# Kernel tuning notes

Measured on AMD Instinct MI355X. Metric: run time of the kernel, lower is better.

Reference implementation:

```python
import jax, jax.numpy as jnp
import numpy as np

B, T, F, U = 256, 1024, 64, 128  # batch, history_size, model_input_num, GRU units


def gru(x_seq, W, Uk, b, return_sequences):
    """Keras GRU (reset_after=True, recurrent_activation=sigmoid, activation=relu).
    x_seq: [B,T,F_in]; W: [F_in,3U]; Uk: [U,3U]; b: [2,3U] (input bias, recurrent bias).
    """
    b_i, b_r = b[0], b[1]
    xw = jnp.einsum('bti,iu->btu', x_seq, W) + b_i  # precompute input projection [B,T,3U]

    def step(h, xw_t):
        rec = h @ Uk + b_r                          # [B,3U]
        xz, xr, xh = jnp.split(xw_t, 3, axis=-1)
        rz, rr, rh = jnp.split(rec, 3, axis=-1)
        z = jax.nn.sigmoid(xz + rz)
        r = jax.nn.sigmoid(xr + rr)
        hh = jax.nn.relu(xh + r * rh)
        h_new = z * h + (1.0 - z) * hh
        return h_new, h_new

    h0 = jnp.zeros((x_seq.shape[0], Uk.shape[0]), dtype=x_seq.dtype)
    hT, hs = jax.lax.scan(step, h0, jnp.swapaxes(xw, 0, 1))  # scan over time
    if return_sequences:
        return jnp.swapaxes(hs, 0, 1), hT  # [B,T,U], [B,U]
    return hT, hT


def setup_inputs() -> dict:
    key = jax.random.key(0)
    ks = jax.random.split(key, 7)
    s_in1 = 1.0 / np.sqrt(F)
    s_rec = 1.0 / np.sqrt(U)
    return {
        'input_data': jax.random.normal(ks[0], (B, T, F), dtype=jnp.float32),
        'W1': jax.random.normal(ks[1], (F, 3 * U), dtype=jnp.float32) * s_in1,
        'U1': jax.random.normal(ks[2], (U, 3 * U), dtype=jnp.float32) * s_rec,
        'b1': jnp.zeros((2, 3 * U), dtype=jnp.float32),
        'W2': jax.random.normal(ks[3], (U, 3 * U), dtype=jnp.float32) * s_rec,
        'U2': jax.random.normal(ks[4], (U, 3 * U), dtype=jnp.float32) * s_rec,
        'b2': jnp.zeros((2, 3 * U), dtype=jnp.float32),
    }


def reference(input_data, W1, U1, b1, W2, U2, b2):
    seq1, state1 = gru(input_data, W1, U1, b1, return_sequences=True)
    x, state2 = gru(seq1, W2, U2, b2, return_sequences=False)
    return (x, state1, state2)
```

## Files before the change

### kernel.cpp

```cpp
#include <hip/hip_runtime.h>


#define TT 1024
#define FF 64
#define G3 384
#define XW_BYTES (1024ull * 384 * 256 * 2)

typedef __attribute__((ext_vector_type(8))) __bf16 bf16x8;
typedef __attribute__((ext_vector_type(4))) float f32x4;

#define MFMA(a, b, c) __builtin_amdgcn_mfma_f32_16x16x32_bf16((a), (b), (c), 0, 0, 0)

__device__ __forceinline__ float sigf(float x) {
    return __builtin_amdgcn_rcpf(1.0f + __expf(-x));
}

__device__ __forceinline__ f32x4 unpackv(uint2 v) {
    f32x4 o;
    o[0] = __uint_as_float(v.x << 16);
    o[1] = __uint_as_float(v.x & 0xFFFF0000u);
    o[2] = __uint_as_float(v.y << 16);
    o[3] = __uint_as_float(v.y & 0xFFFF0000u);
    return o;
}

__global__ void xw_prepass(
    const float* __restrict__ x, const float* __restrict__ W1,
    const float* __restrict__ b1, unsigned short* __restrict__ ws)
{
    const int tid = threadIdx.x, wave = tid >> 6, lane = tid & 63;
    const int quad = lane >> 4, lc = lane & 15;
    const int rb = blockIdx.x;
    const int t  = blockIdx.y * 4 + wave;

    const float* px = x + ((size_t)(rb * 16 + lc) * TT + t) * FF + quad * 8;
    f32x4 u0 = *(const f32x4*)px;
    f32x4 u1 = *(const f32x4*)(px + 4);
    f32x4 u2 = *(const f32x4*)(px + 32);
    f32x4 u3 = *(const f32x4*)(px + 36);
    bf16x8 xa0, xa1;
#pragma unroll
    for (int j = 0; j < 4; j++) {
        xa0[j] = (__bf16)u0[j]; xa0[j + 4] = (__bf16)u1[j];
        xa1[j] = (__bf16)u2[j]; xa1[j + 4] = (__bf16)u3[j];
    }

    uint2* wq = (uint2*)ws + ((size_t)t * 16 + rb) * 1536 + lane;
    for (int nt = 0; nt < 24; nt++) {
        const int g  = nt >> 3;
        const int cg = nt & 7;
        const int uc = cg * 16 + lc;
        float bi = b1[g * 128 + uc];
        if (g < 2) bi += b1[G3 + g * 128 + uc];
        bf16x8 w0, w1v;
#pragma unroll
        for (int j = 0; j < 8; j++) {
            w0[j]  = (__bf16)W1[(quad * 8 + j) * G3 + g * 128 + uc];
            w1v[j] = (__bf16)W1[(32 + quad * 8 + j) * G3 + g * 128 + uc];
        }
        f32x4 acc = {bi, bi, bi, bi};
        acc = MFMA(xa0, w0, acc);
        acc = MFMA(xa1, w1v, acc);
        unsigned int s0 = __builtin_bit_cast(unsigned short, (__bf16)acc[0]);
        unsigned int s1 = __builtin_bit_cast(unsigned short, (__bf16)acc[1]);
        unsigned int s2 = __builtin_bit_cast(unsigned short, (__bf16)acc[2]);
        unsigned int s3 = __builtin_bit_cast(unsigned short, (__bf16)acc[3]);
        uint2 st;
        st.x = s0 | (s1 << 16);
        st.y = s2 | (s3 << 16);
        wq[(size_t)(g * 8 + cg) * 64] = st;
    }
}

template <bool PRE>
__global__ __launch_bounds__(512, 2) void gru_persist(
    const float* __restrict__ x,  const float* __restrict__ W1,
    const float* __restrict__ U1, const float* __restrict__ b1,
    const float* __restrict__ W2, const float* __restrict__ U2,
    const float* __restrict__ b2, const unsigned short* __restrict__ xw,
    float* __restrict__ out)
{
    const int tid  = threadIdx.x;
    const int wave = tid >> 6;
    const int lane = tid & 63;
    const int quad = lane >> 4;
    const int lc   = lane & 15;
    const int row0 = blockIdx.x * 16;
    const int u    = wave * 16 + lc;

    __shared__ __align__(16) __bf16 h1s[2][16][136];
    __shared__ __align__(16) __bf16 h2s[2][16][136];
    for (int i = tid; i < 2 * 16 * 136; i += 512) {
        ((__bf16*)h1s)[i] = (__bf16)0.f;
        ((__bf16*)h2s)[i] = (__bf16)0.f;
    }

    bf16x8 U1B[3][4], W2B[3][4], U2B[3][4];
    bf16x8 W1B[3][2];
#pragma unroll
    for (int g = 0; g < 3; g++) {
#pragma unroll
        for (int kt = 0; kt < 4; kt++) {
            bf16x8 a, b, c;
#pragma unroll
            for (int j = 0; j < 8; j++) {
                int k = (kt * 32 + quad * 8 + j) * G3 + g * 128 + u;
                a[j] = (__bf16)U1[k];
                b[j] = (__bf16)W2[k];
                c[j] = (__bf16)U2[k];
            }
            U1B[g][kt] = a;
            W2B[g][kt] = b;
            U2B[g][kt] = c;
        }
        if constexpr (!PRE) {
#pragma unroll
            for (int kt = 0; kt < 2; kt++) {
                bf16x8 a;
#pragma unroll
                for (int j = 0; j < 8; j++)
                    a[j] = (__bf16)W1[(kt * 32 + quad * 8 + j) * G3 + g * 128 + u];
                W1B[g][kt] = a;
            }
        }
    }

    float c1z  = b1[u] + b1[G3 + u];
    float c1r  = b1[128 + u] + b1[G3 + 128 + u];
    float b1ih = b1[256 + u];
    float b1rh = b1[G3 + 256 + u];
    float c2z  = b2[u] + b2[G3 + u];
    float c2r  = b2[128 + u] + b2[G3 + 128 + u];
    float b2ih = b2[256 + u];
    float b2rh = b2[G3 + 256 + u];

    const uint2* xqb = (const uint2*)xw + (size_t)blockIdx.x * 1536
                       + wave * 64 + lane;
    uint2 xwv[3];
    if constexpr (PRE) {
#pragma unroll
        for (int g = 0; g < 3; g++)
            xwv[g] = xqb[(size_t)g * 512];
    }
    const float* xrow = x + (size_t)(row0 + lc) * (TT * FF) + quad * 8;

    float h1c[4] = {0, 0, 0, 0};
    float h2c[4] = {0, 0, 0, 0};

    __syncthreads();

#define STEP(T, PAR)                                                           \
    {                                                                          \
        bf16x8 A1[4];                                                          \
        _Pragma("unroll") for (int kt = 0; kt < 4; kt++)                       \
            A1[kt] = *(const bf16x8*)&h1s[PAR ^ 1][lc][kt * 32 + quad * 8];    \
        f32x4 z1, r1, rh1, xh1;                                                \
        if constexpr (PRE) {                                                   \
            z1  = unpackv(xwv[0]);                   \
            r1  = unpackv(xwv[1]);                                             \
            xh1 = unpackv(xwv[2]);                    \
            rh1 = (f32x4){b1rh, b1rh, b1rh, b1rh};                             \
            if ((T) + 1 < TT) {                                                \
                _Pragma("unroll") for (int g = 0; g < 3; g++)                  \
                    xwv[g] = xqb[(size_t)((T) + 1) * 24576 + g * 512];         \
            }                                                                  \
        } else {                                                               \
            const float* px = xrow + (size_t)(T) * FF;                         \
            f32x4 u0 = *(const f32x4*)px;                                      \
            f32x4 u1 = *(const f32x4*)(px + 4);                                \
            f32x4 u2 = *(const f32x4*)(px + 32);                               \
            f32x4 u3 = *(const f32x4*)(px + 36);                               \
            bf16x8 xa0, xa1;                                                   \
            _Pragma("unroll") for (int j = 0; j < 4; j++) {                    \
                xa0[j] = (__bf16)u0[j]; xa0[j + 4] = (__bf16)u1[j];            \
                xa1[j] = (__bf16)u2[j]; xa1[j + 4] = (__bf16)u3[j];            \
            }                                                                  \
            z1  = (f32x4){c1z, c1z, c1z, c1z};                                 \
            r1  = (f32x4){c1r, c1r, c1r, c1r};                                 \
            rh1 = (f32x4){b1rh, b1rh, b1rh, b1rh};                             \
            xh1 = (f32x4){b1ih, b1ih, b1ih, b1ih};                             \
            z1  = MFMA(xa0, W1B[0][0], z1);                                    \
            z1  = MFMA(xa1, W1B[0][1], z1);                                    \
            r1  = MFMA(xa0, W1B[1][0], r1);                                    \
            r1  = MFMA(xa1, W1B[1][1], r1);                                    \
            xh1 = MFMA(xa0, W1B[2][0], xh1);                                   \
            xh1 = MFMA(xa1, W1B[2][1], xh1);                                   \
        }                                                                      \
        _Pragma("unroll") for (int kt = 0; kt < 4; kt++) {                     \
            z1  = MFMA(A1[kt], U1B[0][kt], z1);                                \
            r1  = MFMA(A1[kt], U1B[1][kt], r1);                                \
            rh1 = MFMA(A1[kt], U1B[2][kt], rh1);                               \
        }                                                                      \
        _Pragma("unroll") for (int i = 0; i < 4; i++) {                        \
            float zf = sigf(z1[i]);                                            \
            float rf = sigf(r1[i]);                                            \
            float hh = fmaxf(xh1[i] + rf * rh1[i], 0.f);                       \
            h1c[i] = fmaf(zf, h1c[i] - hh, hh);                                \
            h1s[PAR][quad * 4 + i][u] = (__bf16)h1c[i];                        \
        }                                                                      \
        f32x4 z2  = (f32x4){c2z, c2z, c2z, c2z};                               \
        f32x4 r2  = (f32x4){c2r, c2r, c2r, c2r};                               \
        f32x4 xh2 = (f32x4){b2ih, b2ih, b2ih, b2ih};                           \
        f32x4 rh2 = (f32x4){b2rh, b2rh, b2rh, b2rh};                           \
        _Pragma("unroll") for (int kt = 0; kt < 4; kt++) {                     \
            z2  = MFMA(A1[kt], W2B[0][kt], z2);                                \
            r2  = MFMA(A1[kt], W2B[1][kt], r2);                                \
            xh2 = MFMA(A1[kt], W2B[2][kt], xh2);                               \
        }                                                                      \
        _Pragma("unroll") for (int kt = 0; kt < 4; kt++) {                     \
            bf16x8 A2 = *(const bf16x8*)&h2s[PAR][lc][kt * 32 + quad * 8];     \
            z2  = MFMA(A2, U2B[0][kt], z2);                                    \
            r2  = MFMA(A2, U2B[1][kt], r2);                                    \
            rh2 = MFMA(A2, U2B[2][kt], rh2);                                   \
        }                                                                      \
        if ((T) > 0) {                                                         \
            _Pragma("unroll") for (int i = 0; i < 4; i++) {                    \
                float zf = sigf(z2[i]);                                        \
                float rf = sigf(r2[i]);                                        \
                float hh = fmaxf(xh2[i] + rf * rh2[i], 0.f);                   \
                h2c[i] = fmaf(zf, h2c[i] - hh, hh);                            \
            }                                                                  \
        }                                                                      \
        _Pragma("unroll") for (int i = 0; i < 4; i++)                          \
            h2s[PAR ^ 1][quad * 4 + i][u] = (__bf16)h2c[i];                    \
        asm volatile("s_waitcnt lgkmcnt(0)\n\ts_barrier" ::: "memory");        \
    }

    for (int t = 0; t < TT; t += 2) {
        STEP(t, 0)
        STEP(t + 1, 1)
    }
#undef STEP

    {
        f32x4 z2  = (f32x4){c2z, c2z, c2z, c2z};
        f32x4 r2  = (f32x4){c2r, c2r, c2r, c2r};
        f32x4 xh2 = (f32x4){b2ih, b2ih, b2ih, b2ih};
        f32x4 rh2 = (f32x4){b2rh, b2rh, b2rh, b2rh};
#pragma unroll
        for (int kt = 0; kt < 4; kt++) {
            bf16x8 a1 = *(const bf16x8*)&h1s[1][lc][kt * 32 + quad * 8];
            bf16x8 a2 = *(const bf16x8*)&h2s[0][lc][kt * 32 + quad * 8];
            z2  = MFMA(a1, W2B[0][kt], z2);
            r2  = MFMA(a1, W2B[1][kt], r2);
            xh2 = MFMA(a1, W2B[2][kt], xh2);
            z2  = MFMA(a2, U2B[0][kt], z2);
            r2  = MFMA(a2, U2B[1][kt], r2);
            rh2 = MFMA(a2, U2B[2][kt], rh2);
        }
#pragma unroll
        for (int i = 0; i < 4; i++) {
            float zf = sigf(z2[i]);
            float rf = sigf(r2[i]);
            float hh = fmaxf(xh2[i] + rf * rh2[i], 0.f);
            h2c[i] = fmaf(zf, h2c[i] - hh, hh);
        }
    }

#pragma unroll
    for (int i = 0; i < 4; i++) {
        int r = row0 + quad * 4 + i;
        out[(size_t)r * 128 + u]         = h2c[i];
        out[32768 + (size_t)r * 128 + u] = h1c[i];
        out[65536 + (size_t)r * 128 + u] = h2c[i];
    }
}

extern "C" void kernel_launch(void* const* d_in, const int* in_sizes, int n_in,
                              void* d_out, int out_size, void* d_ws, size_t ws_size,
                              hipStream_t stream) {
    const float* x  = (const float*)d_in[0];
    const float* W1 = (const float*)d_in[1];
    const float* U1 = (const float*)d_in[2];
    const float* b1 = (const float*)d_in[3];
    const float* W2 = (const float*)d_in[4];
    const float* U2 = (const float*)d_in[5];
    const float* b2 = (const float*)d_in[6];
    float* out = (float*)d_out;

    if (ws_size >= XW_BYTES) {
        unsigned short* ws = (unsigned short*)d_ws;
        xw_prepass<<<dim3(16, 256), dim3(256), 0, stream>>>(x, W1, b1, ws);
        gru_persist<true><<<dim3(16), dim3(512), 0, stream>>>(
            x, W1, U1, b1, W2, U2, b2, ws, out);
    } else {
        gru_persist<false><<<dim3(16), dim3(512), 0, stream>>>(
            x, W1, U1, b1, W2, U2, b2, nullptr, out);
    }
}
```

Measured before the change: 1.247 ms.

## Specialize waves per GRU layer in a 12-wave pipelined persistent kernel

The persistent kernel now launches 768 threads and dedicates 4 waves to layer 1 (each handling 32 units) and 8 waves to layer 2, so the two layers compute concurrently. Layer 2 at step t consumes layer-1 output from step t-1, which makes the layers a software pipeline with one barrier per step. The aim is to shorten the serial per-step critical path, which previously ran layer 1 then layer 2 in every wave. The cost is a skewed schedule that needs an extra final layer-2 step, higher register pressure on the layer-1 waves, and imbalanced MFMA work between the two wave groups. The fallback path also seeds MFMA accumulators directly with bias vectors.

```diff
diff --git a/kernel.cpp b/kernel.cpp
--- a/kernel.cpp
+++ b/kernel.cpp
@@ -72,9 +72,9 @@
     }
 }
 
-template <bool PRE>
-__global__ __launch_bounds__(512, 2) void gru_persist(
-    const float* __restrict__ x,  const float* __restrict__ W1,
+__global__ __launch_bounds__(768)
+__attribute__((amdgpu_waves_per_eu(3)))
+void gru_persist(
     const float* __restrict__ U1, const float* __restrict__ b1,
     const float* __restrict__ W2, const float* __restrict__ U2,
     const float* __restrict__ b2, const unsigned short* __restrict__ xw,
@@ -86,6 +86,207 @@
     const int quad = lane >> 4;
     const int lc   = lane & 15;
     const int row0 = blockIdx.x * 16;
+    const bool isL1 = wave < 4;
+
+    __shared__ __align__(16) __bf16 h1s[2][16][136];
+    __shared__ __align__(16) __bf16 h2s[2][16][136];
+    for (int i = tid; i < 2 * 16 * 136; i += 768) {
+        ((__bf16*)h1s)[i] = (__bf16)0.f;
+        ((__bf16*)h2s)[i] = (__bf16)0.f;
+    }
+
+    bf16x8 WB[2][3][4];
+    f32x4 bq[4];
+    uint2 xwv[2][3];
+    const uint2* xqb = (const uint2*)xw + (size_t)blockIdx.x * 1536
+                       + (size_t)(wave * 2) * 64 + lane;
+
+    if (isL1) {
+#pragma unroll
+        for (int gg = 0; gg < 2; gg++) {
+            const int uc = wave * 32 + gg * 16 + lc;
+#pragma unroll
+            for (int g = 0; g < 3; g++)
+#pragma unroll
+                for (int kt = 0; kt < 4; kt++) {
+                    bf16x8 a;
+#pragma unroll
+                    for (int j = 0; j < 8; j++)
+                        a[j] = (__bf16)U1[(kt * 32 + quad * 8 + j) * G3 + g * 128 + uc];
+                    WB[gg][g][kt] = a;
+                }
+            float b = b1[G3 + 256 + uc];
+            bq[gg] = (f32x4){b, b, b, b};
+        }
+#pragma unroll
+        for (int gg = 0; gg < 2; gg++)
+#pragma unroll
+            for (int g = 0; g < 3; g++)
+                xwv[gg][g] = xqb[(size_t)g * 512 + gg * 64];
+    } else {
+        const int uc = (wave - 4) * 16 + lc;
+#pragma unroll
+        for (int g = 0; g < 3; g++)
+#pragma unroll
+            for (int kt = 0; kt < 4; kt++) {
+                bf16x8 b, c;
+#pragma unroll
+                for (int j = 0; j < 8; j++) {
+                    int k = (kt * 32 + quad * 8 + j) * G3 + g * 128 + uc;
+                    b[j] = (__bf16)W2[k];
+                    c[j] = (__bf16)U2[k];
+                }
+                WB[0][g][kt] = b;
+                WB[1][g][kt] = c;
+            }
+        float v0 = b2[uc] + b2[G3 + uc];
+        float v1 = b2[128 + uc] + b2[G3 + 128 + uc];
+        float v2 = b2[256 + uc];
+        float v3 = b2[G3 + 256 + uc];
+        bq[0] = (f32x4){v0, v0, v0, v0};
+        bq[1] = (f32x4){v1, v1, v1, v1};
+        bq[2] = (f32x4){v2, v2, v2, v2};
+        bq[3] = (f32x4){v3, v3, v3, v3};
+    }
+
+    float hc[2][4] = {{0, 0, 0, 0}, {0, 0, 0, 0}};
+    __syncthreads();
+
+#define STEP(T, PAR)                                                           \
+    {                                                                          \
+        if (isL1) {                                                            \
+            _Pragma("unroll") for (int gg = 0; gg < 2; gg++) {                 \
+                f32x4 z1  = unpackv(xwv[gg][0]);                               \
+                f32x4 r1  = unpackv(xwv[gg][1]);                               \
+                f32x4 xh1 = unpackv(xwv[gg][2]);                               \
+                if ((T) + 1 < TT) {                                            \
+                    _Pragma("unroll") for (int g = 0; g < 3; g++)              \
+                        xwv[gg][g] =                                           \
+                            xqb[(size_t)((T) + 1) * 24576 + g * 512 + gg * 64];\
+                }                                                              \
+                f32x4 rh1;                                                     \
+                {                                                              \
+                    bf16x8 A = *(const bf16x8*)&h1s[PAR ^ 1][lc][quad * 8];    \
+                    rh1 = MFMA(A, WB[gg][2][0], bq[gg]);                       \
+                    z1  = MFMA(A, WB[gg][0][0], z1);                           \
+                    r1  = MFMA(A, WB[gg][1][0], r1);                           \
+                }                                                              \
+                _Pragma("unroll") for (int kt = 1; kt < 4; kt++) {             \
+                    bf16x8 A =                                                 \
+                        *(const bf16x8*)&h1s[PAR ^ 1][lc][kt * 32 + quad * 8]; \
+                    z1  = MFMA(A, WB[gg][0][kt], z1);                          \
+                    r1  = MFMA(A, WB[gg][1][kt], r1);                          \
+                    rh1 = MFMA(A, WB[gg][2][kt], rh1);                         \
+                }                                                              \
+                const int uc = wave * 32 + gg * 16 + lc;                       \
+                _Pragma("unroll") for (int i = 0; i < 4; i++) {                \
+                    float zf = sigf(z1[i]);                                    \
+                    float rf = sigf(r1[i]);                                    \
+                    float hh = fmaxf(xh1[i] + rf * rh1[i], 0.f);               \
+                    hc[gg][i] = fmaf(zf, hc[gg][i] - hh, hh);                  \
+                    h1s[PAR][quad * 4 + i][uc] = (__bf16)hc[gg][i];            \
+                }                                                              \
+            }                                                                  \
+        } else {                                                               \
+            f32x4 z2, r2, xh2, rh2;                                            \
+            {                                                                  \
+                bf16x8 A = *(const bf16x8*)&h1s[PAR ^ 1][lc][quad * 8];        \
+                z2  = MFMA(A, WB[0][0][0], bq[0]);                             \
+                r2  = MFMA(A, WB[0][1][0], bq[1]);                             \
+                xh2 = MFMA(A, WB[0][2][0], bq[2]);                             \
+            }                                                                  \
+            _Pragma("unroll") for (int kt = 1; kt < 4; kt++) {                 \
+                bf16x8 A =                                                     \
+                    *(const bf16x8*)&h1s[PAR ^ 1][lc][kt * 32 + quad * 8];     \
+                z2  = MFMA(A, WB[0][0][kt], z2);                               \
+                r2  = MFMA(A, WB[0][1][kt], r2);                               \
+                xh2 = MFMA(A, WB[0][2][kt], xh2);                              \
+            }                                                                  \
+            {                                                                  \
+                bf16x8 A = *(const bf16x8*)&h2s[PAR ^ 1][lc][quad * 8];        \
+                rh2 = MFMA(A, WB[1][2][0], bq[3]);                             \
+                z2  = MFMA(A, WB[1][0][0], z2);                                \
+                r2  = MFMA(A, WB[1][1][0], r2);                                \
+            }                                                                  \
+            _Pragma("unroll") for (int kt = 1; kt < 4; kt++) {                 \
+                bf16x8 A =                                                     \
+                    *(const bf16x8*)&h2s[PAR ^ 1][lc][kt * 32 + quad * 8];     \
+                z2  = MFMA(A, WB[1][0][kt], z2);                               \
+                r2  = MFMA(A, WB[1][1][kt], r2);                               \
+                rh2 = MFMA(A, WB[1][2][kt], rh2);                              \
+            }                                                                  \
+            if ((T) > 0) {                                                     \
+                _Pragma("unroll") for (int i = 0; i < 4; i++) {                \
+                    float zf = sigf(z2[i]);                                    \
+                    float rf = sigf(r2[i]);                                    \
+                    float hh = fmaxf(xh2[i] + rf * rh2[i], 0.f);               \
+                    hc[0][i] = fmaf(zf, hc[0][i] - hh, hh);                    \
+                }                                                              \
+            }                                                                  \
+            const int uc = (wave - 4) * 16 + lc;                               \
+            _Pragma("unroll") for (int i = 0; i < 4; i++)                      \
+                h2s[PAR][quad * 4 + i][uc] = (__bf16)hc[0][i];                 \
+        }                                                                      \
+        asm volatile("s_waitcnt lgkmcnt(0)\n\ts_barrier" ::: "memory");        \
+    }
+
+    for (int t = 0; t < TT; t += 2) {
+        STEP(t, 0)
+        STEP(t + 1, 1)
+    }
+#undef STEP
+
+    if (isL1) {
+#pragma unroll
+        for (int gg = 0; gg < 2; gg++) {
+            const int uc = wave * 32 + gg * 16 + lc;
+#pragma unroll
+            for (int i = 0; i < 4; i++) {
+                int r = row0 + quad * 4 + i;
+                out[32768 + (size_t)r * 128 + uc] = hc[gg][i];
+            }
+        }
+    } else {
+        f32x4 z2 = bq[0], r2 = bq[1], xh2 = bq[2], rh2 = bq[3];
+#pragma unroll
+        for (int kt = 0; kt < 4; kt++) {
+            bf16x8 a1 = *(const bf16x8*)&h1s[1][lc][kt * 32 + quad * 8];
+            bf16x8 a2 = *(const bf16x8*)&h2s[1][lc][kt * 32 + quad * 8];
+            z2  = MFMA(a1, WB[0][0][kt], z2);
+            r2  = MFMA(a1, WB[0][1][kt], r2);
+            xh2 = MFMA(a1, WB[0][2][kt], xh2);
+            z2  = MFMA(a2, WB[1][0][kt], z2);
+            r2  = MFMA(a2, WB[1][1][kt], r2);
+            rh2 = MFMA(a2, WB[1][2][kt], rh2);
+        }
+        const int uc = (wave - 4) * 16 + lc;
+#pragma unroll
+        for (int i = 0; i < 4; i++) {
+            float zf = sigf(z2[i]);
+            float rf = sigf(r2[i]);
+            float hh = fmaxf(xh2[i] + rf * rh2[i], 0.f);
+            float h2 = fmaf(zf, hc[0][i] - hh, hh);
+            int r = row0 + quad * 4 + i;
+            out[(size_t)r * 128 + uc]         = h2;
+            out[65536 + (size_t)r * 128 + uc] = h2;
+        }
+    }
+}
+
+__global__ __launch_bounds__(512)
+__attribute__((amdgpu_waves_per_eu(2, 2)))
+void gru_mono(
+    const float* __restrict__ x,  const float* __restrict__ W1,
+    const float* __restrict__ U1, const float* __restrict__ b1,
+    const float* __restrict__ W2, const float* __restrict__ U2,
+    const float* __restrict__ b2, float* __restrict__ out)
+{
+    const int tid  = threadIdx.x;
+    const int wave = tid >> 6;
+    const int lane = tid & 63;
+    const int quad = lane >> 4;
+    const int lc   = lane & 15;
+    const int row0 = blockIdx.x * 16;
     const int u    = wave * 16 + lc;
 
     __shared__ __align__(16) __bf16 h1s[2][16][136];
@@ -95,8 +296,7 @@
         ((__bf16*)h2s)[i] = (__bf16)0.f;
     }
 
-    bf16x8 U1B[3][4], W2B[3][4], U2B[3][4];
-    bf16x8 W1B[3][2];
+    bf16x8 U1B[3][4], W2B[3][4], U2B[3][4], W1B[3][2];
 #pragma unroll
     for (int g = 0; g < 3; g++) {
 #pragma unroll
@@ -109,84 +309,65 @@
                 b[j] = (__bf16)W2[k];
                 c[j] = (__bf16)U2[k];
             }
-            U1B[g][kt] = a;
-            W2B[g][kt] = b;
-            U2B[g][kt] = c;
-        }
-        if constexpr (!PRE) {
-#pragma unroll
-            for (int kt = 0; kt < 2; kt++) {
-                bf16x8 a;
-#pragma unroll
-                for (int j = 0; j < 8; j++)
-                    a[j] = (__bf16)W1[(kt * 32 + quad * 8 + j) * G3 + g * 128 + u];
-                W1B[g][kt] = a;
-            }
-        }
-    }
-
-    float c1z  = b1[u] + b1[G3 + u];
-    float c1r  = b1[128 + u] + b1[G3 + 128 + u];
-    float b1ih = b1[256 + u];
-    float b1rh = b1[G3 + 256 + u];
-    float c2z  = b2[u] + b2[G3 + u];
-    float c2r  = b2[128 + u] + b2[G3 + 128 + u];
-    float b2ih = b2[256 + u];
-    float b2rh = b2[G3 + 256 + u];
-
-    const uint2* xqb = (const uint2*)xw + (size_t)blockIdx.x * 1536
-                       + wave * 64 + lane;
-    uint2 xwv[3];
-    if constexpr (PRE) {
-#pragma unroll
-        for (int g = 0; g < 3; g++)
-            xwv[g] = xqb[(size_t)g * 512];
-    }
+            U1B[g][kt] = a; W2B[g][kt] = b; U2B[g][kt] = c;
+        }
+#pragma unroll
+        for (int kt = 0; kt < 2; kt++) {
+            bf16x8 a;
+#pragma unroll
+            for (int j = 0; j < 8; j++)
+                a[j] = (__bf16)W1[(kt * 32 + quad * 8 + j) * G3 + g * 128 + u];
+            W1B[g][kt] = a;
+        }
+    }
+
+    const float c1z  = b1[u] + b1[G3 + u];
+    const float c1r  = b1[128 + u] + b1[G3 + 128 + u];
+    const float b1ih = b1[256 + u];
+    const float b1rh = b1[G3 + 256 + u];
+    const float c2z  = b2[u] + b2[G3 + u];
+    const float c2r  = b2[128 + u] + b2[G3 + 128 + u];
+    const float b2ih = b2[256 + u];
+    const float b2rh = b2[G3 + 256 + u];
+    const f32x4 c1zq  = {c1z, c1z, c1z, c1z};
+    const f32x4 c1rq  = {c1r, c1r, c1r, c1r};
+    const f32x4 b1ihq = {b1ih, b1ih, b1ih, b1ih};
+    const f32x4 b1rhq = {b1rh, b1rh, b1rh, b1rh};
+    const f32x4 c2zq  = {c2z, c2z, c2z, c2z};
+    const f32x4 c2rq  = {c2r, c2r, c2r, c2r};
+    const f32x4 b2ihq = {b2ih, b2ih, b2ih, b2ih};
+    const f32x4 b2rhq = {b2rh, b2rh, b2rh, b2rh};
+
     const float* xrow = x + (size_t)(row0 + lc) * (TT * FF) + quad * 8;
-
     float h1c[4] = {0, 0, 0, 0};
     float h2c[4] = {0, 0, 0, 0};
-
     __syncthreads();
 
-#define STEP(T, PAR)                                                           \
+#define MSTEP(T, PAR)                                                          \
     {                                                                          \
         bf16x8 A1[4];                                                          \
         _Pragma("unroll") for (int kt = 0; kt < 4; kt++)                       \
             A1[kt] = *(const bf16x8*)&h1s[PAR ^ 1][lc][kt * 32 + quad * 8];    \
-        f32x4 z1, r1, rh1, xh1;                                                \
-        if constexpr (PRE) {                                                   \
-            z1  = unpackv(xwv[0]);                   \
-            r1  = unpackv(xwv[1]);                                             \
-            xh1 = unpackv(xwv[2]);                    \
-            rh1 = (f32x4){b1rh, b1rh, b1rh, b1rh};                             \
-            if ((T) + 1 < TT) {                                                \
-                _Pragma("unroll") for (int g = 0; g < 3; g++)                  \
-                    xwv[g] = xqb[(size_t)((T) + 1) * 24576 + g * 512];         \
-            }                                                                  \
-        } else {                                                               \
-            const float* px = xrow + (size_t)(T) * FF;                         \
-            f32x4 u0 = *(const f32x4*)px;                                      \
-            f32x4 u1 = *(const f32x4*)(px + 4);                                \
-            f32x4 u2 = *(const f32x4*)(px + 32);                               \
-            f32x4 u3 = *(const f32x4*)(px + 36);                               \
-            bf16x8 xa0, xa1;                                                   \
-            _Pragma("unroll") for (int j = 0; j < 4; j++) {                    \
-                xa0[j] = (__bf16)u0[j]; xa0[j + 4] = (__bf16)u1[j];            \
-                xa1[j] = (__bf16)u2[j]; xa1[j + 4] = (__bf16)u3[j];            \
-            }                                                                  \
-            z1  = (f32x4){c1z, c1z, c1z, c1z};                                 \
-            r1  = (f32x4){c1r, c1r, c1r, c1r};                                 \
-            rh1 = (f32x4){b1rh, b1rh, b1rh, b1rh};                             \
-            xh1 = (f32x4){b1ih, b1ih, b1ih, b1ih};                             \
-            z1  = MFMA(xa0, W1B[0][0], z1);                                    \
-            z1  = MFMA(xa1, W1B[0][1], z1);                                    \
-            r1  = MFMA(xa0, W1B[1][0], r1);                                    \
-            r1  = MFMA(xa1, W1B[1][1], r1);                                    \
-            xh1 = MFMA(xa0, W1B[2][0], xh1);                                   \
-            xh1 = MFMA(xa1, W1B[2][1], xh1);                                   \
-        }                                                                      \
-        _Pragma("unroll") for (int kt = 0; kt < 4; kt++) {                     \
+        const float* px = xrow + (size_t)(T) * FF;                             \
+        f32x4 u0 = *(const f32x4*)px;                                          \
+        f32x4 u1 = *(const f32x4*)(px + 4);                                    \
+        f32x4 u2 = *(const f32x4*)(px + 32);                                   \
+        f32x4 u3 = *(const f32x4*)(px + 36);                                   \
+        bf16x8 xa0, xa1;                                                       \
+        _Pragma("unroll") for (int j = 0; j < 4; j++) {                        \
+            xa0[j] = (__bf16)u0[j]; xa0[j + 4] = (__bf16)u1[j];                \
+            xa1[j] = (__bf16)u2[j]; xa1[j + 4] = (__bf16)u3[j];                \
+        }                                                                      \
+        f32x4 z1  = MFMA(xa0, W1B[0][0], c1zq);                                \
+        z1        = MFMA(xa1, W1B[0][1], z1);                                  \
+        f32x4 r1  = MFMA(xa0, W1B[1][0], c1rq);                                \
+        r1        = MFMA(xa1, W1B[1][1], r1);                                  \
+        f32x4 xh1 = MFMA(xa0, W1B[2][0], b1ihq);                               \
+        xh1       = MFMA(xa1, W1B[2][1], xh1);                                 \
+        f32x4 rh1 = MFMA(A1[0], U1B[2][0], b1rhq);                             \
+        z1        = MFMA(A1[0], U1B[0][0], z1);                                \
+        r1        = MFMA(A1[0], U1B[1][0], r1);                                \
+        _Pragma("unroll") for (int kt = 1; kt < 4; kt++) {                     \
             z1  = MFMA(A1[kt], U1B[0][kt], z1);                                \
             r1  = MFMA(A1[kt], U1B[1][kt], r1);                                \
             rh1 = MFMA(A1[kt], U1B[2][kt], rh1);                               \
@@ -198,16 +379,22 @@
             h1c[i] = fmaf(zf, h1c[i] - hh, hh);                                \
             h1s[PAR][quad * 4 + i][u] = (__bf16)h1c[i];                        \
         }                                                                      \
-        f32x4 z2  = (f32x4){c2z, c2z, c2z, c2z};                               \
-        f32x4 r2  = (f32x4){c2r, c2r, c2r, c2r};                               \
-        f32x4 xh2 = (f32x4){b2ih, b2ih, b2ih, b2ih};                           \
-        f32x4 rh2 = (f32x4){b2rh, b2rh, b2rh, b2rh};                           \
-        _Pragma("unroll") for (int kt = 0; kt < 4; kt++) {                     \
+        f32x4 z2  = MFMA(A1[0], W2B[0][0], c2zq);                              \
+        f32x4 r2  = MFMA(A1[0], W2B[1][0], c2rq);                              \
+        f32x4 xh2 = MFMA(A1[0], W2B[2][0], b2ihq);                             \
+        _Pragma("unroll") for (int kt = 1; kt < 4; kt++) {                     \
             z2  = MFMA(A1[kt], W2B[0][kt], z2);                                \
             r2  = MFMA(A1[kt], W2B[1][kt], r2);                                \
             xh2 = MFMA(A1[kt], W2B[2][kt], xh2);                               \
         }                                                                      \
-        _Pragma("unroll") for (int kt = 0; kt < 4; kt++) {                     \
+        f32x4 rh2;                                                             \
+        {                                                                      \
+            bf16x8 A2 = *(const bf16x8*)&h2s[PAR][lc][quad * 8];               \
+            rh2 = MFMA(A2, U2B[2][0], b2rhq);                                  \
+            z2  = MFMA(A2, U2B[0][0], z2);                                     \
+            r2  = MFMA(A2, U2B[1][0], r2);                                     \
+        }                                                                      \
+        _Pragma("unroll") for (int kt = 1; kt < 4; kt++) {                     \
             bf16x8 A2 = *(const bf16x8*)&h2s[PAR][lc][kt * 32 + quad * 8];     \
             z2  = MFMA(A2, U2B[0][kt], z2);                                    \
             r2  = MFMA(A2, U2B[1][kt], r2);                                    \
@@ -227,16 +414,13 @@
     }
 
     for (int t = 0; t < TT; t += 2) {
-        STEP(t, 0)
-        STEP(t + 1, 1)
-    }
-#undef STEP
+        MSTEP(t, 0)
+        MSTEP(t + 1, 1)
+    }
+#undef MSTEP
 
     {
-        f32x4 z2  = (f32x4){c2z, c2z, c2z, c2z};
-        f32x4 r2  = (f32x4){c2r, c2r, c2r, c2r};
-        f32x4 xh2 = (f32x4){b2ih, b2ih, b2ih, b2ih};
-        f32x4 rh2 = (f32x4){b2rh, b2rh, b2rh, b2rh};
+        f32x4 z2 = c2zq, r2 = c2rq, xh2 = b2ihq, rh2 = b2rhq;
 #pragma unroll
         for (int kt = 0; kt < 4; kt++) {
             bf16x8 a1 = *(const bf16x8*)&h1s[1][lc][kt * 32 + quad * 8];
@@ -281,10 +465,10 @@
     if (ws_size >= XW_BYTES) {
         unsigned short* ws = (unsigned short*)d_ws;
         xw_prepass<<<dim3(16, 256), dim3(256), 0, stream>>>(x, W1, b1, ws);
-        gru_persist<true><<<dim3(16), dim3(512), 0, stream>>>(
-            x, W1, U1, b1, W2, U2, b2, ws, out);
+        gru_persist<<<dim3(16), dim3(768), 0, stream>>>(
+            U1, b1, W2, U2, b2, ws, out);
     } else {
-        gru_persist<false><<<dim3(16), dim3(512), 0, stream>>>(
-            x, W1, U1, b1, W2, U2, b2, nullptr, out);
-    }
-}
+        gru_mono<<<dim3(16), dim3(512), 0, stream>>>(
+            x, W1, U1, b1, W2, U2, b2, out);
+    }
+}
```

Result: slower. 2.010 ms (+61.2%).

## Fuse layer-1 input projection into persistent GRU kernel with prefetched x

Applied to the files above, without the earlier changes.

Removes the separate xw prepass kernel and its bf16 workspace round-trip, computing the layer-1 input projection with MFMA inside the persistent recurrent kernel instead. The next timestep's x row is prefetched into registers one step ahead to hide global load latency, and bias vectors are folded in as MFMA accumulator initial values. This saves a kernel launch and the write/read of a large intermediate, but adds six MFMAs per step to the serial critical path of the recurrence.

```diff
diff --git a/kernel.cpp b/kernel.cpp
--- a/kernel.cpp
+++ b/kernel.cpp
@@ -4,7 +4,6 @@
 #define TT 1024
 #define FF 64
 #define G3 384
-#define XW_BYTES (1024ull * 384 * 256 * 2)
 
 typedef __attribute__((ext_vector_type(8))) __bf16 bf16x8;
 typedef __attribute__((ext_vector_type(4))) float f32x4;
@@ -15,70 +14,13 @@
     return __builtin_amdgcn_rcpf(1.0f + __expf(-x));
 }
 
-__device__ __forceinline__ f32x4 unpackv(uint2 v) {
-    f32x4 o;
-    o[0] = __uint_as_float(v.x << 16);
-    o[1] = __uint_as_float(v.x & 0xFFFF0000u);
-    o[2] = __uint_as_float(v.y << 16);
-    o[3] = __uint_as_float(v.y & 0xFFFF0000u);
-    return o;
-}
-
-__global__ void xw_prepass(
-    const float* __restrict__ x, const float* __restrict__ W1,
-    const float* __restrict__ b1, unsigned short* __restrict__ ws)
-{
-    const int tid = threadIdx.x, wave = tid >> 6, lane = tid & 63;
-    const int quad = lane >> 4, lc = lane & 15;
-    const int rb = blockIdx.x;
-    const int t  = blockIdx.y * 4 + wave;
-
-    const float* px = x + ((size_t)(rb * 16 + lc) * TT + t) * FF + quad * 8;
-    f32x4 u0 = *(const f32x4*)px;
-    f32x4 u1 = *(const f32x4*)(px + 4);
-    f32x4 u2 = *(const f32x4*)(px + 32);
-    f32x4 u3 = *(const f32x4*)(px + 36);
-    bf16x8 xa0, xa1;
-#pragma unroll
-    for (int j = 0; j < 4; j++) {
-        xa0[j] = (__bf16)u0[j]; xa0[j + 4] = (__bf16)u1[j];
-        xa1[j] = (__bf16)u2[j]; xa1[j + 4] = (__bf16)u3[j];
-    }
-
-    uint2* wq = (uint2*)ws + ((size_t)t * 16 + rb) * 1536 + lane;
-    for (int nt = 0; nt < 24; nt++) {
-        const int g  = nt >> 3;
-        const int cg = nt & 7;
-        const int uc = cg * 16 + lc;
-        float bi = b1[g * 128 + uc];
-        if (g < 2) bi += b1[G3 + g * 128 + uc];
-        bf16x8 w0, w1v;
-#pragma unroll
-        for (int j = 0; j < 8; j++) {
-            w0[j]  = (__bf16)W1[(quad * 8 + j) * G3 + g * 128 + uc];
-            w1v[j] = (__bf16)W1[(32 + quad * 8 + j) * G3 + g * 128 + uc];
-        }
-        f32x4 acc = {bi, bi, bi, bi};
-        acc = MFMA(xa0, w0, acc);
-        acc = MFMA(xa1, w1v, acc);
-        unsigned int s0 = __builtin_bit_cast(unsigned short, (__bf16)acc[0]);
-        unsigned int s1 = __builtin_bit_cast(unsigned short, (__bf16)acc[1]);
-        unsigned int s2 = __builtin_bit_cast(unsigned short, (__bf16)acc[2]);
-        unsigned int s3 = __builtin_bit_cast(unsigned short, (__bf16)acc[3]);
-        uint2 st;
-        st.x = s0 | (s1 << 16);
-        st.y = s2 | (s3 << 16);
-        wq[(size_t)(g * 8 + cg) * 64] = st;
-    }
-}
-
-template <bool PRE>
-__global__ __launch_bounds__(512, 2) void gru_persist(
+__global__ __launch_bounds__(512)
+__attribute__((amdgpu_waves_per_eu(2, 2)))
+void gru_mono(
     const float* __restrict__ x,  const float* __restrict__ W1,
     const float* __restrict__ U1, const float* __restrict__ b1,
     const float* __restrict__ W2, const float* __restrict__ U2,
-    const float* __restrict__ b2, const unsigned short* __restrict__ xw,
-    float* __restrict__ out)
+    const float* __restrict__ b2, float* __restrict__ out)
 {
     const int tid  = threadIdx.x;
     const int wave = tid >> 6;
@@ -95,8 +37,7 @@
         ((__bf16*)h2s)[i] = (__bf16)0.f;
     }
 
-    bf16x8 U1B[3][4], W2B[3][4], U2B[3][4];
-    bf16x8 W1B[3][2];
+    bf16x8 U1B[3][4], W2B[3][4], U2B[3][4], W1B[3][2];
 #pragma unroll
     for (int g = 0; g < 3; g++) {
 #pragma unroll
@@ -109,84 +50,72 @@
                 b[j] = (__bf16)W2[k];
                 c[j] = (__bf16)U2[k];
             }
-            U1B[g][kt] = a;
-            W2B[g][kt] = b;
-            U2B[g][kt] = c;
-        }
-        if constexpr (!PRE) {
-#pragma unroll
-            for (int kt = 0; kt < 2; kt++) {
-                bf16x8 a;
-#pragma unroll
-                for (int j = 0; j < 8; j++)
-                    a[j] = (__bf16)W1[(kt * 32 + quad * 8 + j) * G3 + g * 128 + u];
-                W1B[g][kt] = a;
-            }
-        }
-    }
-
-    float c1z  = b1[u] + b1[G3 + u];
-    float c1r  = b1[128 + u] + b1[G3 + 128 + u];
-    float b1ih = b1[256 + u];
-    float b1rh = b1[G3 + 256 + u];
-    float c2z  = b2[u] + b2[G3 + u];
-    float c2r  = b2[128 + u] + b2[G3 + 128 + u];
-    float b2ih = b2[256 + u];
-    float b2rh = b2[G3 + 256 + u];
-
-    const uint2* xqb = (const uint2*)xw + (size_t)blockIdx.x * 1536
-                       + wave * 64 + lane;
-    uint2 xwv[3];
-    if constexpr (PRE) {
-#pragma unroll
-        for (int g = 0; g < 3; g++)
-            xwv[g] = xqb[(size_t)g * 512];
-    }
+            U1B[g][kt] = a; W2B[g][kt] = b; U2B[g][kt] = c;
+        }
+#pragma unroll
+        for (int kt = 0; kt < 2; kt++) {
+            bf16x8 a;
+#pragma unroll
+            for (int j = 0; j < 8; j++)
+                a[j] = (__bf16)W1[(kt * 32 + quad * 8 + j) * G3 + g * 128 + u];
+            W1B[g][kt] = a;
+        }
+    }
+
+    const float c1z  = b1[u] + b1[G3 + u];
+    const float c1r  = b1[128 + u] + b1[G3 + 128 + u];
+    const float b1ih = b1[256 + u];
+    const float b1rh = b1[G3 + 256 + u];
+    const float c2z  = b2[u] + b2[G3 + u];
+    const float c2r  = b2[128 + u] + b2[G3 + 128 + u];
+    const float b2ih = b2[256 + u];
+    const float b2rh = b2[G3 + 256 + u];
+    const f32x4 c1zq  = {c1z, c1z, c1z, c1z};
+    const f32x4 c1rq  = {c1r, c1r, c1r, c1r};
+    const f32x4 b1ihq = {b1ih, b1ih, b1ih, b1ih};
+    const f32x4 b1rhq = {b1rh, b1rh, b1rh, b1rh};
+    const f32x4 c2zq  = {c2z, c2z, c2z, c2z};
+    const f32x4 c2rq  = {c2r, c2r, c2r, c2r};
+    const f32x4 b2ihq = {b2ih, b2ih, b2ih, b2ih};
+    const f32x4 b2rhq = {b2rh, b2rh, b2rh, b2rh};
+
     const float* xrow = x + (size_t)(row0 + lc) * (TT * FF) + quad * 8;
+    f32x4 xp0 = *(const f32x4*)(xrow);
+    f32x4 xp1 = *(const f32x4*)(xrow + 4);
+    f32x4 xp2 = *(const f32x4*)(xrow + 32);
+    f32x4 xp3 = *(const f32x4*)(xrow + 36);
 
     float h1c[4] = {0, 0, 0, 0};
     float h2c[4] = {0, 0, 0, 0};
-
     __syncthreads();
 
-#define STEP(T, PAR)                                                           \
+#define MSTEP(T, PAR)                                                          \
     {                                                                          \
         bf16x8 A1[4];                                                          \
         _Pragma("unroll") for (int kt = 0; kt < 4; kt++)                       \
             A1[kt] = *(const bf16x8*)&h1s[PAR ^ 1][lc][kt * 32 + quad * 8];    \
-        f32x4 z1, r1, rh1, xh1;                                                \
-        if constexpr (PRE) {                                                   \
-            z1  = unpackv(xwv[0]);                   \
-            r1  = unpackv(xwv[1]);                                             \
-            xh1 = unpackv(xwv[2]);                    \
-            rh1 = (f32x4){b1rh, b1rh, b1rh, b1rh};                             \
-            if ((T) + 1 < TT) {                                                \
-                _Pragma("unroll") for (int g = 0; g < 3; g++)                  \
-                    xwv[g] = xqb[(size_t)((T) + 1) * 24576 + g * 512];         \
-            }                                                                  \
-        } else {                                                               \
-            const float* px = xrow + (size_t)(T) * FF;                         \
-            f32x4 u0 = *(const f32x4*)px;                                      \
-            f32x4 u1 = *(const f32x4*)(px + 4);                                \
-            f32x4 u2 = *(const f32x4*)(px + 32);                               \
-            f32x4 u3 = *(const f32x4*)(px + 36);                               \
-            bf16x8 xa0, xa1;                                                   \
-            _Pragma("unroll") for (int j = 0; j < 4; j++) {                    \
-                xa0[j] = (__bf16)u0[j]; xa0[j + 4] = (__bf16)u1[j];            \
-                xa1[j] = (__bf16)u2[j]; xa1[j + 4] = (__bf16)u3[j];            \
-            }                                                                  \
-            z1  = (f32x4){c1z, c1z, c1z, c1z};                                 \
-            r1  = (f32x4){c1r, c1r, c1r, c1r};                                 \
-            rh1 = (f32x4){b1rh, b1rh, b1rh, b1rh};                             \
-            xh1 = (f32x4){b1ih, b1ih, b1ih, b1ih};                             \
-            z1  = MFMA(xa0, W1B[0][0], z1);                                    \
-            z1  = MFMA(xa1, W1B[0][1], z1);                                    \
-            r1  = MFMA(xa0, W1B[1][0], r1);                                    \
-            r1  = MFMA(xa1, W1B[1][1], r1);                                    \
-            xh1 = MFMA(xa0, W1B[2][0], xh1);                                   \
-            xh1 = MFMA(xa1, W1B[2][1], xh1);                                   \
-        }                                                                      \
-        _Pragma("unroll") for (int kt = 0; kt < 4; kt++) {                     \
+        bf16x8 xa0, xa1;                                                       \
+        _Pragma("unroll") for (int j = 0; j < 4; j++) {                        \
+            xa0[j] = (__bf16)xp0[j]; xa0[j + 4] = (__bf16)xp1[j];              \
+            xa1[j] = (__bf16)xp2[j]; xa1[j + 4] = (__bf16)xp3[j];              \
+        }                                                                      \
+        if ((T) + 1 < TT) {                               \
+            const float* px = xrow + (size_t)((T) + 1) * FF;                   \
+            xp0 = *(const f32x4*)px;                                           \
+            xp1 = *(const f32x4*)(px + 4);                                     \
+            xp2 = *(const f32x4*)(px + 32);                                    \
+            xp3 = *(const f32x4*)(px + 36);                                    \
+        }                                                                      \
+        f32x4 z1  = MFMA(xa0, W1B[0][0], c1zq);                                \
+        z1        = MFMA(xa1, W1B[0][1], z1);                                  \
+        f32x4 r1  = MFMA(xa0, W1B[1][0], c1rq);                                \
+        r1        = MFMA(xa1, W1B[1][1], r1);                                  \
+        f32x4 xh1 = MFMA(xa0, W1B[2][0], b1ihq);                               \
+        xh1       = MFMA(xa1, W1B[2][1], xh1);                                 \
+        f32x4 rh1 = MFMA(A1[0], U1B[2][0], b1rhq);                             \
+        z1        = MFMA(A1[0], U1B[0][0], z1);                                \
+        r1        = MFMA(A1[0], U1B[1][0], r1);                                \
+        _Pragma("unroll") for (int kt = 1; kt < 4; kt++) {                     \
             z1  = MFMA(A1[kt], U1B[0][kt], z1);                                \
             r1  = MFMA(A1[kt], U1B[1][kt], r1);                                \
             rh1 = MFMA(A1[kt], U1B[2][kt], rh1);                               \
@@ -198,16 +127,22 @@
             h1c[i] = fmaf(zf, h1c[i] - hh, hh);                                \
             h1s[PAR][quad * 4 + i][u] = (__bf16)h1c[i];                        \
         }                                                                      \
-        f32x4 z2  = (f32x4){c2z, c2z, c2z, c2z};                               \
-        f32x4 r2  = (f32x4){c2r, c2r, c2r, c2r};                               \
-        f32x4 xh2 = (f32x4){b2ih, b2ih, b2ih, b2ih};                           \
-        f32x4 rh2 = (f32x4){b2rh, b2rh, b2rh, b2rh};                           \
-        _Pragma("unroll") for (int kt = 0; kt < 4; kt++) {                     \
+        f32x4 z2  = MFMA(A1[0], W2B[0][0], c2zq);                              \
+        f32x4 r2  = MFMA(A1[0], W2B[1][0], c2rq);                              \
+        f32x4 xh2 = MFMA(A1[0], W2B[2][0], b2ihq);                             \
+        _Pragma("unroll") for (int kt = 1; kt < 4; kt++) {                     \
             z2  = MFMA(A1[kt], W2B[0][kt], z2);                                \
             r2  = MFMA(A1[kt], W2B[1][kt], r2);                                \
             xh2 = MFMA(A1[kt], W2B[2][kt], xh2);                               \
         }                                                                      \
-        _Pragma("unroll") for (int kt = 0; kt < 4; kt++) {                     \
+        f32x4 rh2;                                                             \
+        {                                                                      \
+            bf16x8 A2 = *(const bf16x8*)&h2s[PAR][lc][quad * 8];               \
+            rh2 = MFMA(A2, U2B[2][0], b2rhq);                                  \
+            z2  = MFMA(A2, U2B[0][0], z2);                                     \
+            r2  = MFMA(A2, U2B[1][0], r2);                                     \
+        }                                                                      \
+        _Pragma("unroll") for (int kt = 1; kt < 4; kt++) {                     \
             bf16x8 A2 = *(const bf16x8*)&h2s[PAR][lc][kt * 32 + quad * 8];     \
             z2  = MFMA(A2, U2B[0][kt], z2);                                    \
             r2  = MFMA(A2, U2B[1][kt], r2);                                    \
@@ -227,16 +162,13 @@
     }
 
     for (int t = 0; t < TT; t += 2) {
-        STEP(t, 0)
-        STEP(t + 1, 1)
-    }
-#undef STEP
+        MSTEP(t, 0)
+        MSTEP(t + 1, 1)
+    }
+#undef MSTEP
 
     {
-        f32x4 z2  = (f32x4){c2z, c2z, c2z, c2z};
-        f32x4 r2  = (f32x4){c2r, c2r, c2r, c2r};
-        f32x4 xh2 = (f32x4){b2ih, b2ih, b2ih, b2ih};
-        f32x4 rh2 = (f32x4){b2rh, b2rh, b2rh, b2rh};
+        f32x4 z2 = c2zq, r2 = c2rq, xh2 = b2ihq, rh2 = b2rhq;
 #pragma unroll
         for (int kt = 0; kt < 4; kt++) {
             bf16x8 a1 = *(const bf16x8*)&h1s[1][lc][kt * 32 + quad * 8];
@@ -278,13 +210,6 @@
     const float* b2 = (const float*)d_in[6];
     float* out = (float*)d_out;
 
-    if (ws_size >= XW_BYTES) {
-        unsigned short* ws = (unsigned short*)d_ws;
-        xw_prepass<<<dim3(16, 256), dim3(256), 0, stream>>>(x, W1, b1, ws);
-        gru_persist<true><<<dim3(16), dim3(512), 0, stream>>>(
-            x, W1, U1, b1, W2, U2, b2, ws, out);
-    } else {
-        gru_persist<false><<<dim3(16), dim3(512), 0, stream>>>(
-            x, W1, U1, b1, W2, U2, b2, nullptr, out);
-    }
+    gru_mono<<<dim3(16), dim3(512), 0, stream>>>(
+        x, W1, U1, b1, W2, U2, b2, out);
 }
```

Measured after the change: 3.443 ms. +176.2%, slower.
